# Optimization experiments

Measured on AMD Instinct MI355X. Metric: run time of the kernel, lower is better.

Reference implementation:

```python
import jax, jax.numpy as jnp
import numpy as np

N = 50000   # nodes
E = 800000  # edges (avg degree 16)
H = 64      # hidden feature dim (hidden_irreps = 64x0e)
A = 9       # attr dim = (lmax_attr+1)^2, lmax_attr=2
AMF = 1     # additional_message_features dim
L = 2       # num_layers (stacked SEGNNLayers)


def _swish(v):
    return v * jax.nn.sigmoid(v)


def _o3_tp(v, attr, W, V, b):
    # Channel-factorized (uvu-style) attribute-conditioned tensor product:
    # linear map of features, gated per-channel by a linear map of the
    # steerable attribute (spherical harmonics), plus bias.
    return (v @ W) * (attr @ V) + b


def setup_inputs() -> dict:
    key = jax.random.key(0)
    ks = jax.random.split(key, 18)
    sc = lambda fan_in: 1.0 / np.sqrt(fan_in)
    inp = {
        "x": jax.random.normal(ks[0], (N, H), jnp.float32),
        "edge_attr": jax.random.normal(ks[1], (E, A), jnp.float32),
        "node_attr": jax.random.normal(ks[2], (N, A), jnp.float32),
        "amf": jax.random.normal(ks[3], (E, AMF), jnp.float32),
        "Wm1": jax.random.normal(ks[4], (L, 2 * H + AMF, H), jnp.float32) * sc(2 * H + AMF),
        "Vm1": jax.random.normal(ks[5], (L, A, H), jnp.float32) * sc(A),
        "bm1": jnp.zeros((L, H), jnp.float32),
        "Wm2": jax.random.normal(ks[6], (L, H, H), jnp.float32) * sc(H),
        "Vm2": jax.random.normal(ks[7], (L, A, H), jnp.float32) * sc(A),
        "bm2": jnp.zeros((L, H), jnp.float32),
        "Wu1": jax.random.normal(ks[8], (L, 2 * H, H), jnp.float32) * sc(2 * H),
        "Vu1": jax.random.normal(ks[9], (L, A, H), jnp.float32) * sc(A),
        "bu1": jnp.zeros((L, H), jnp.float32),
        "Wu2": jax.random.normal(ks[10], (L, H, H), jnp.float32) * sc(H),
        "Vu2": jax.random.normal(ks[11], (L, A, H), jnp.float32) * sc(A),
        "bu2": jnp.zeros((L, H), jnp.float32),
        "edge_index": jax.random.randint(ks[12], (2, E), 0, N, jnp.int64),
    }
    return inp


def reference(x, edge_attr, node_attr, amf,
              Wm1, Vm1, bm1, Wm2, Vm2, bm2,
              Wu1, Vu1, bu1, Wu2, Vu2, bu2,
              edge_index):
    src = edge_index[0]  # x_j source
    dst = edge_index[1]  # x_i target / aggregation index
    for l in range(L):
        # --- message: gather, concat, TP-SwishGate x2 ---
        x_i = x[dst]                                   # [E, H]
        x_j = x[src]                                   # [E, H]
        m_in = jnp.concatenate([x_i, x_j, amf], -1)    # [E, 2H+AMF]
        m = _swish(_o3_tp(m_in, edge_attr, Wm1[l], Vm1[l], bm1[l]))
        m = _swish(_o3_tp(m, edge_attr, Wm2[l], Vm2[l], bm2[l]))
        # --- aggregate: scatter-add messages to target nodes ---
        agg = jax.ops.segment_sum(m, dst, num_segments=N)  # [N, H]
        # --- update: concat, TP-SwishGate, TP, residual blend ---
        u_in = jnp.concatenate([x, agg], -1)           # [N, 2H]
        u = _swish(_o3_tp(u_in, node_attr, Wu1[l], Vu1[l], bu1[l]))
        u = _o3_tp(u, node_attr, Wu2[l], Vu2[l], bu2[l])
        x = 0.7 * x + 0.3 * u
    return x
```

## Files before the change

### kernel.cpp

```cpp
#include <hip/hip_runtime.h>
#include <hip/hip_bf16.h>

#define NN 50000
#define NE 800000
#define H  64
#define AD 9

typedef __attribute__((ext_vector_type(8)))  short short8;
typedef __attribute__((ext_vector_type(16))) float f32x16;
typedef unsigned int uint;
typedef unsigned short ushort;

union U8 { short8 v; uint u[4]; ushort s[8]; };

__device__ __forceinline__ f32x16 MFMA(short8 a, short8 b, f32x16 c) {
    return __builtin_amdgcn_mfma_f32_32x32x16_bf16(a, b, c, 0, 0, 0);
}

__device__ __forceinline__ ushort f2bf(float v) {
    __hip_bfloat16 b = __float2bfloat16(v);
    return *(ushort*)&b;
}
__device__ __forceinline__ uint pkbf(float a, float b) {
    uint r;
    asm volatile("v_cvt_pk_bf16_f32 %0, %1, %2" : "=v"(r) : "v"(a), "v"(b));
    return r;
}
__device__ __forceinline__ float bflo(uint u) { return __uint_as_float(u << 16); }
__device__ __forceinline__ float bfhi(uint u) { return __uint_as_float(u & 0xffff0000u); }

__device__ __forceinline__ float swish_fast(float v) {
    return v * __builtin_amdgcn_rcpf(1.f + __expf(-v));
}

__device__ __forceinline__ void xhalf(uint& a, uint& b) {
    asm("v_permlane32_swap_b32 %0, %1" : "+v"(a), "+v"(b));
}

__device__ __forceinline__ void pack16(const float* y, short8* out) {
    #pragma unroll
    for (int g = 0; g < 2; ++g) {
        uint c0 = pkbf(y[g*8+0], y[g*8+1]);
        uint c1 = pkbf(y[g*8+2], y[g*8+3]);
        uint c2 = pkbf(y[g*8+4], y[g*8+5]);
        uint c3 = pkbf(y[g*8+6], y[g*8+7]);
        xhalf(c0, c2);
        xhalf(c1, c3);
        U8 q; q.u[0] = c0; q.u[1] = c1; q.u[2] = c2; q.u[3] = c3;
        out[g] = q.v;
    }
}

__global__ void prep_x(const float* __restrict__ x, ushort* __restrict__ xb) {
    int t = blockIdx.x * 256 + threadIdx.x;
    if (t >= NN * H / 8) return;
    const float* p = x + (size_t)t * 8;
    U8 o;
    #pragma unroll
    for (int j = 0; j < 8; ++j) o.s[j] = f2bf(p[j]);
    *(short8*)(xb + (size_t)t * 8) = o.v;
}

__global__ void prep_w(const float* __restrict__ Wm1, const float* __restrict__ Vm1,
                       const float* __restrict__ Wm2, const float* __restrict__ Vm2,
                       const float* __restrict__ Wu1, const float* __restrict__ Vu1,
                       const float* __restrict__ Wu2, const float* __restrict__ Vu2,
                       ushort* __restrict__ wbE, ushort* __restrict__ wbN) {
    int t = blockIdx.x * 256 + threadIdx.x;
    float v = 0.f;
    if (t < 2 * 17408) {
        int l = t / 17408, o = t % 17408;
        if (o < 10752)      { int h = o / 168, k = o % 168;            if (k < 129) v = Wm1[l*8256 + k*64 + h]; }
        else if (o < 15360) { int o2 = o-10752; int h = o2/72, k = o2%72; if (k < 64)  v = Wm2[l*4096 + k*64 + h]; }
        else if (o < 16384) { int o2 = o-15360; int h = o2/16, a = o2%16; if (a < 9)   v = Vm1[l*576 + a*64 + h]; }
        else                { int o2 = o-16384; int h = o2/16, a = o2%16; if (a < 9)   v = Vm2[l*576 + a*64 + h]; }
        wbE[t] = f2bf(v);
    } else if (t < 2 * 17408 + 2 * 15360) {
        int u = t - 2 * 17408;
        int l = u / 15360, o = u % 15360;
        if (o < 8704)       { int h = o / 136, k = o % 136;            if (k < 128) v = Wu1[l*8192 + k*64 + h]; }
        else if (o < 13312) { int o2 = o-8704;  int h = o2/72, k = o2%72; if (k < 64)  v = Wu2[l*4096 + k*64 + h]; }
        else if (o < 14336) { int o2 = o-13312; int h = o2/16, a = o2%16; if (a < 9)   v = Vu1[l*576 + a*64 + h]; }
        else                { int o2 = o-14336; int h = o2/16, a = o2%16; if (a < 9)   v = Vu2[l*576 + a*64 + h]; }
        wbN[u] = f2bf(v);
    }
}

__global__ void hist_k(const int* __restrict__ ei, int* __restrict__ cnt) {
    int t = blockIdx.x * 256 + threadIdx.x;
    if (t < NE) atomicAdd(&cnt[ei[NE + t]], 1);
}

__global__ void scan1_k(const int* __restrict__ cnt, int* __restrict__ partial,
                        int* __restrict__ btot) {
    __shared__ int sh[256];
    const int b = blockIdx.x, tid = threadIdx.x, i = b * 256 + tid;
    int c = cnt[i];
    sh[tid] = c; __syncthreads();
    int run = c;
    for (int off = 1; off < 256; off <<= 1) {
        int t = (tid >= off) ? sh[tid - off] : 0;
        __syncthreads();
        run += t; sh[tid] = run; __syncthreads();
    }
    partial[i] = run - c;
    if (tid == 255) btot[b] = run;
}

__global__ void scan2_k(const int* __restrict__ btot, int* __restrict__ boff) {
    __shared__ int sh[256];
    const int tid = threadIdx.x;
    int c = (tid < 200) ? btot[tid] : 0;
    sh[tid] = c; __syncthreads();
    int run = c;
    for (int off = 1; off < 256; off <<= 1) {
        int t = (tid >= off) ? sh[tid - off] : 0;
        __syncthreads();
        run += t; sh[tid] = run; __syncthreads();
    }
    boff[tid] = run - c;
}

__global__ void scan3_k(const int* __restrict__ partial, const int* __restrict__ boff,
                        int* __restrict__ cursor) {
    int b = blockIdx.x, i = b * 256 + threadIdx.x;
    if (i < NN) cursor[i] = partial[i] + boff[b];
}

__global__ void fill_k(const int* __restrict__ ei, const float* __restrict__ edge_attr,
                       const float* __restrict__ amf, int* __restrict__ cursor,
                       int* __restrict__ srcS, int* __restrict__ dstS,
                       uint4* __restrict__ eaLo, uint2* __restrict__ eaHi) {
    int e = blockIdx.x * 256 + threadIdx.x;
    if (e >= NE) return;
    const int dst = ei[NE + e], src = ei[e];
    const int pos = atomicAdd(&cursor[dst], 1);
    srcS[pos] = src; dstS[pos] = dst;
    float ea[AD];
    #pragma unroll
    for (int a = 0; a < AD; ++a) ea[a] = edge_attr[(size_t)e * AD + a];
    uint4 lo;
    lo.x = pkbf(ea[0], ea[1]); lo.y = pkbf(ea[2], ea[3]);
    lo.z = pkbf(ea[4], ea[5]); lo.w = pkbf(ea[6], ea[7]);
    eaLo[pos] = lo;
    uint2 hw;
    hw.x = pkbf(ea[8], 0.f); hw.y = pkbf(amf[e], 0.f);
    eaHi[pos] = hw;
}

struct M2Pack { short8 v[4]; };

__device__ __forceinline__ M2Pack msg_compute(
    const short8 bx[8], uint4 elo, uint2 ehi,
    const ushort* __restrict__ W1T, const ushort* __restrict__ wb,
    const short8 aW2[4][2], const short8 aV1[2], const short8 aV2[2],
    const float* __restrict__ b1, const float* __restrict__ b2,
    int l31, int hi) {
    U8 bea;
    bea.u[0] = hi ? ehi.x : elo.x;
    bea.u[1] = hi ? 0u : elo.y;
    bea.u[2] = hi ? 0u : elo.z;
    bea.u[3] = hi ? 0u : elo.w;

    f32x16 gA0 = {}, gA1 = {};
    gA0 = MFMA(aV1[0], bea.v, gA0);
    gA1 = MFMA(aV1[1], bea.v, gA1);

    f32x16 mA0 = {}, mA1 = {};
    #pragma unroll
    for (int s = 0; s < 8; ++s) {
        short8 a0 = *(const short8*)(W1T + l31 * 168 + s * 16 + hi * 8);
        short8 a1 = *(const short8*)(W1T + (l31 + 32) * 168 + s * 16 + hi * 8);
        mA0 = MFMA(a0, bx[s], mA0);
        mA1 = MFMA(a1, bx[s], mA1);
    }
    {
        U8 ba;
        ba.u[0] = hi ? 0u : ehi.y;
        ba.u[1] = 0; ba.u[2] = 0; ba.u[3] = 0;
        short8 a0 = *(const short8*)(W1T + l31 * 168 + 128 + hi * 8);
        short8 a1 = *(const short8*)(W1T + (l31 + 32) * 168 + 128 + hi * 8);
        mA0 = MFMA(a0, ba.v, mA0);
        mA1 = MFMA(a1, ba.v, mA1);
    }

    short8 bm[4];
    #pragma unroll
    for (int m = 0; m < 2; ++m) {
        const f32x16 mc = m ? mA1 : mA0;
        const f32x16 gc = m ? gA1 : gA0;
        float y[16];
        #pragma unroll
        for (int r = 0; r < 16; ++r) {
            int h0 = (r & 3) + 8 * (r >> 2) + 32 * m;
            float bb = hi ? b1[h0 + 4] : b1[h0];
            y[r] = swish_fast(fmaf(mc[r], gc[r], bb));
        }
        pack16(y, &bm[2 * m]);
    }

    f32x16 h0a = {}, h1a = {};
    h0a = MFMA(aV2[0], bea.v, h0a);
    h1a = MFMA(aV2[1], bea.v, h1a);
    f32x16 p0 = {}, p1 = {};
    #pragma unroll
    for (int s = 0; s < 4; ++s) {
        p0 = MFMA(aW2[s][0], bm[s], p0);
        p1 = MFMA(aW2[s][1], bm[s], p1);
    }

    M2Pack out;
    #pragma unroll
    for (int m = 0; m < 2; ++m) {
        const f32x16 mc = m ? p1 : p0;
        const f32x16 gc = m ? h1a : h0a;
        float y[16];
        #pragma unroll
        for (int r = 0; r < 16; ++r) {
            int h0 = (r & 3) + 8 * (r >> 2) + 32 * m;
            float bb = hi ? b2[h0 + 4] : b2[h0];
            y[r] = swish_fast(fmaf(mc[r], gc[r], bb));
        }
        pack16(y, &out.v[2 * m]);
    }
    return out;
}

__device__ __forceinline__ void gather_x(short8 bx[8], const ushort* __restrict__ xbf,
                                         int dst, int src, int hi) {
    const ushort* xd = xbf + (size_t)dst * H;
    const ushort* xs = xbf + (size_t)src * H;
    #pragma unroll
    for (int s = 0; s < 8; ++s)
        bx[s] = *(const short8*)((s < 4 ? xd : xs) + (s & 3) * 16 + hi * 8);
}

__device__ __forceinline__ void seg_reduce(const ushort* __restrict__ M2, int dst,
                                           float* __restrict__ agg, int lane) {
    float acc = 0.f;
    int cur = __builtin_amdgcn_readlane(dst, 0);
    #pragma unroll
    for (int r = 0; r < 32; ++r) {
        float v = bflo((uint)M2[r * 68 + lane]);
        int d = __builtin_amdgcn_readlane(dst, r);
        if (d != cur) {
            atomicAdd(&agg[(size_t)cur * H + lane], acc);
            acc = 0.f; cur = d;
        }
        acc += v;
    }
    atomicAdd(&agg[(size_t)cur * H + lane], acc);
}

__global__ __launch_bounds__(256, 4) void edge_mfma(
    const ushort* __restrict__ xbf, const uint4* __restrict__ eaLo,
    const uint2* __restrict__ eaHi, const int* __restrict__ srcS,
    const int* __restrict__ dstS, const ushort* __restrict__ wb,
    const float* __restrict__ b1, const float* __restrict__ b2,
    float* __restrict__ agg) {
    __shared__ __align__(16) ushort lds[10752 + 4 * 32 * 68];
    {
        const uint4* s4 = (const uint4*)wb;
        uint4* d4 = (uint4*)lds;
        for (int i = threadIdx.x; i < 1344; i += 256) d4[i] = s4[i];
    }
    __syncthreads();
    const ushort* W1T = lds;

    const int lane = threadIdx.x & 63;
    const int wv   = threadIdx.x >> 6;
    const int hi   = lane >> 5;
    const int l31  = lane & 31;
    ushort* M2 = lds + 10752 + wv * (32 * 68);

    const int i0 = blockIdx.x * 256 + wv * 64 + l31;
    const int i1 = i0 + 32;

    const int dst0 = dstS[i0], src0 = srcS[i0];
    const int dst1 = dstS[i1], src1 = srcS[i1];
    const uint4 elo0 = eaLo[i0], elo1 = eaLo[i1];
    const uint2 ehi0 = eaHi[i0], ehi1 = eaHi[i1];

    short8 aW2[4][2], aV1[2], aV2[2];
    #pragma unroll
    for (int m = 0; m < 2; ++m) {
        int r = l31 + 32 * m;
        aV1[m] = *(const short8*)(wb + 15360 + r * 16 + hi * 8);
        aV2[m] = *(const short8*)(wb + 16384 + r * 16 + hi * 8);
        #pragma unroll
        for (int s = 0; s < 4; ++s)
            aW2[s][m] = *(const short8*)(wb + 10752 + r * 72 + s * 16 + hi * 8);
    }

    short8 bx0[8];
    gather_x(bx0, xbf, dst0, src0, hi);
    M2Pack p0 = msg_compute(bx0, elo0, ehi0, W1T, wb, aW2, aV1, aV2, b1, b2, l31, hi);

    short8 bx1[8];
    gather_x(bx1, xbf, dst1, src1, hi);

    #pragma unroll
    for (int j = 0; j < 4; ++j)
        *(short8*)(M2 + l31 * 68 + j * 16 + hi * 8) = p0.v[j];
    seg_reduce(M2, dst0, agg, lane);

    M2Pack p1 = msg_compute(bx1, elo1, ehi1, W1T, wb, aW2, aV1, aV2, b1, b2, l31, hi);
    #pragma unroll
    for (int j = 0; j < 4; ++j)
        *(short8*)(M2 + l31 * 68 + j * 16 + hi * 8) = p1.v[j];
    seg_reduce(M2, dst1, agg, lane);
}

__global__ __launch_bounds__(256, 4) void node_mfma(
    const ushort* __restrict__ xbf, const float* __restrict__ agg,
    const float* __restrict__ node_attr, const ushort* __restrict__ wb,
    const float* __restrict__ b1, const float* __restrict__ b2,
    ushort* __restrict__ xnext, float* __restrict__ outf, int last) {
    __shared__ __align__(16) ushort lds[8704];
    {
        const uint4* s4 = (const uint4*)wb;
        uint4* d4 = (uint4*)lds;
        for (int i = threadIdx.x; i < 1088; i += 256) d4[i] = s4[i];
    }
    __syncthreads();
    const ushort* W1T = lds;

    const int lane = threadIdx.x & 63;
    const int wv   = threadIdx.x >> 6;
    const int hi   = lane >> 5;
    const int l31  = lane & 31;
    const int n    = blockIdx.x * 128 + wv * 32 + l31;
    const int nc   = n < NN ? n : NN - 1;

    short8 aW2[4][2], aV1[2], aV2[2];
    #pragma unroll
    for (int m = 0; m < 2; ++m) {
        int r = l31 + 32 * m;
        aV1[m] = *(const short8*)(wb + 13312 + r * 16 + hi * 8);
        aV2[m] = *(const short8*)(wb + 14336 + r * 16 + hi * 8);
        #pragma unroll
        for (int s = 0; s < 4; ++s)
            aW2[s][m] = *(const short8*)(wb + 8704 + r * 72 + s * 16 + hi * 8);
    }

    float na[AD];
    #pragma unroll
    for (int a = 0; a < AD; ++a) na[a] = node_attr[(size_t)nc * AD + a];

    U8 bna;
    {
        uint g0 = pkbf(na[0], na[1]), g1 = pkbf(na[2], na[3]);
        uint g2 = pkbf(na[4], na[5]), g3 = pkbf(na[6], na[7]);
        uint g8 = pkbf(na[8], 0.f);
        bna.u[0] = hi ? g8 : g0;
        bna.u[1] = hi ? 0u : g1;
        bna.u[2] = hi ? 0u : g2;
        bna.u[3] = hi ? 0u : g3;
    }
    f32x16 gA0 = {}, gA1 = {};
    gA0 = MFMA(aV1[0], bna.v, gA0);
    gA1 = MFMA(aV1[1], bna.v, gA1);

    f32x16 mA0 = {}, mA1 = {};
    #pragma unroll
    for (int s = 0; s < 8; ++s) {
        short8 bx;
        if (s < 4) {
            bx = *(const short8*)(xbf + (size_t)nc * H + s * 16 + hi * 8);
        } else {
            const float* ap = agg + (size_t)nc * H + (s - 4) * 16 + hi * 8;
            float4 u0 = *(const float4*)ap;
            float4 u1 = *(const float4*)(ap + 4);
            U8 q;
            q.u[0] = pkbf(u0.x, u0.y); q.u[1] = pkbf(u0.z, u0.w);
            q.u[2] = pkbf(u1.x, u1.y); q.u[3] = pkbf(u1.z, u1.w);
            bx = q.v;
        }
        short8 a0 = *(const short8*)(W1T + l31 * 136 + s * 16 + hi * 8);
        short8 a1 = *(const short8*)(W1T + (l31 + 32) * 136 + s * 16 + hi * 8);
        mA0 = MFMA(a0, bx, mA0);
        mA1 = MFMA(a1, bx, mA1);
    }

    short8 bm[4];
    #pragma unroll
    for (int m = 0; m < 2; ++m) {
        const f32x16 mc = m ? mA1 : mA0;
        const f32x16 gc = m ? gA1 : gA0;
        float y[16];
        #pragma unroll
        for (int r = 0; r < 16; ++r) {
            int h0 = (r & 3) + 8 * (r >> 2) + 32 * m;
            float bb = hi ? b1[h0 + 4] : b1[h0];
            y[r] = swish_fast(fmaf(mc[r], gc[r], bb));
        }
        pack16(y, &bm[2 * m]);
    }

    f32x16 h0a = {}, h1a = {};
    h0a = MFMA(aV2[0], bna.v, h0a);
    h1a = MFMA(aV2[1], bna.v, h1a);
    f32x16 p0 = {}, p1 = {};
    #pragma unroll
    for (int s = 0; s < 4; ++s) {
        p0 = MFMA(aW2[s][0], bm[s], p0);
        p1 = MFMA(aW2[s][1], bm[s], p1);
    }

    #pragma unroll
    for (int m = 0; m < 2; ++m) {
        const f32x16 mc = m ? p1 : p0;
        const f32x16 gc = m ? h1a : h0a;
        float y[16];
        #pragma unroll
        for (int r = 0; r < 16; ++r) {
            int h0 = (r & 3) + 8 * (r >> 2) + 32 * m;
            float bb = hi ? b2[h0 + 4] : b2[h0];
            y[r] = fmaf(mc[r], gc[r], bb);
        }
        #pragma unroll
        for (int g = 0; g < 2; ++g) {
            uint c0 = pkbf(y[g*8+0], y[g*8+1]);
            uint c1 = pkbf(y[g*8+2], y[g*8+3]);
            uint c2 = pkbf(y[g*8+4], y[g*8+5]);
            uint c3 = pkbf(y[g*8+6], y[g*8+7]);
            xhalf(c0, c2);
            xhalf(c1, c3);
            int goff = (2*m + g) * 16 + hi * 8;
            U8 xb; xb.v = *(const short8*)(xbf + (size_t)nc * H + goff);
            float o[8];
            uint cc[4] = {c0, c1, c2, c3};
            #pragma unroll
            for (int j = 0; j < 4; ++j) {
                o[2*j]   = 0.7f * bflo((uint)xb.u[j]) + 0.3f * bflo(cc[j]);
                o[2*j+1] = 0.7f * bfhi((uint)xb.u[j]) + 0.3f * bfhi(cc[j]);
            }
            if (n < NN) {
                if (last) {
                    float4 w0 = {o[0], o[1], o[2], o[3]};
                    float4 w1 = {o[4], o[5], o[6], o[7]};
                    *(float4*)(outf + (size_t)n * H + goff)     = w0;
                    *(float4*)(outf + (size_t)n * H + goff + 4) = w1;
                } else {
                    U8 q;
                    #pragma unroll
                    for (int j = 0; j < 4; ++j) q.u[j] = pkbf(o[2*j], o[2*j+1]);
                    *(short8*)(xnext + (size_t)n * H + goff) = q.v;
                }
            }
        }
    }
}

extern "C" void kernel_launch(void* const* d_in, const int* in_sizes, int n_in,
                              void* d_out, int out_size, void* d_ws, size_t ws_size,
                              hipStream_t stream) {
    const float* x         = (const float*)d_in[0];
    const float* edge_attr = (const float*)d_in[1];
    const float* node_attr = (const float*)d_in[2];
    const float* amf       = (const float*)d_in[3];
    const float* Wm1 = (const float*)d_in[4];
    const float* Vm1 = (const float*)d_in[5];
    const float* bm1 = (const float*)d_in[6];
    const float* Wm2 = (const float*)d_in[7];
    const float* Vm2 = (const float*)d_in[8];
    const float* bm2 = (const float*)d_in[9];
    const float* Wu1 = (const float*)d_in[10];
    const float* Vu1 = (const float*)d_in[11];
    const float* bu1 = (const float*)d_in[12];
    const float* Wu2 = (const float*)d_in[13];
    const float* Vu2 = (const float*)d_in[14];
    const float* bu2 = (const float*)d_in[15];
    const int*   ei  = (const int*)d_in[16];

    float* out = (float*)d_out;
    float* agg = (float*)d_out;

    ushort* xbf0 = (ushort*)d_ws;
    ushort* xbf1 = xbf0 + (size_t)NN * H;
    ushort* wbE  = xbf1 + (size_t)NN * H;
    ushort* wbN  = wbE + 2 * 17408;
    int* cnt     = (int*)(wbN + 2 * 15360);
    int* btot    = cnt + 51200;
    int* boff    = btot + 256;
    int* partial = boff + 256;
    int* cursor  = partial + 51200;
    int* srcS    = cursor + 50048;
    int* dstS    = srcS + NE;
    uint4* eaLo  = (uint4*)(dstS + NE);
    uint2* eaHi  = (uint2*)(eaLo + NE);

    prep_x<<<(NN * H / 8 + 255) / 256, 256, 0, stream>>>(x, xbf0);
    prep_w<<<256, 256, 0, stream>>>(Wm1, Vm1, Wm2, Vm2, Wu1, Vu1, Wu2, Vu2, wbE, wbN);

    hipMemsetAsync(cnt, 0, 51200 * sizeof(int), stream);
    hist_k<<<(NE + 255) / 256, 256, 0, stream>>>(ei, cnt);
    scan1_k<<<200, 256, 0, stream>>>(cnt, partial, btot);
    scan2_k<<<1, 256, 0, stream>>>(btot, boff);
    scan3_k<<<200, 256, 0, stream>>>(partial, boff, cursor);
    fill_k<<<(NE + 255) / 256, 256, 0, stream>>>(ei, edge_attr, amf, cursor,
                                                 srcS, dstS, eaLo, eaHi);

    for (int l = 0; l < 2; ++l) {
        const ushort* xb = (l == 0) ? xbf0 : xbf1;
        hipMemsetAsync(agg, 0, (size_t)NN * H * sizeof(float), stream);
        edge_mfma<<<NE / 256, 256, 0, stream>>>(
            xb, eaLo, eaHi, srcS, dstS, wbE + (size_t)l * 17408,
            bm1 + l * H, bm2 + l * H, agg);
        node_mfma<<<(NN + 127) / 128, 256, 0, stream>>>(
            xb, agg, node_attr, wbN + (size_t)l * 15360,
            bu1 + l * H, bu2 + l * H, xbf1, out, (l == 1) ? 1 : 0);
    }
}
```

Baseline: 312.5 us.

## Register-level segment reduction, packed edge indices, fused prep and XCD swizzle

Transposes the second message MFMA so each lane holds one channel across edges, enabling a ballot-driven in-register segmented sum that replaces the LDS staging buffer and serial reduction. Packs src/dst into ushort2 and edge hi-attributes into one uint to cut index/attribute bandwidth, raises edge-kernel occupancy hint, adds an XCD-aware block remap, and fuses the two prep kernels into one launch. The 16-bit indices rely on node count fitting in 65535, and the per-segment masked sums add ALU work when segments are short.

```diff
diff --git a/kernel.cpp b/kernel.cpp
--- a/kernel.cpp
+++ b/kernel.cpp
@@ -51,22 +51,24 @@
     }
 }
 
-__global__ void prep_x(const float* __restrict__ x, ushort* __restrict__ xb) {
-    int t = blockIdx.x * 256 + threadIdx.x;
-    if (t >= NN * H / 8) return;
-    const float* p = x + (size_t)t * 8;
-    U8 o;
-    #pragma unroll
-    for (int j = 0; j < 8; ++j) o.s[j] = f2bf(p[j]);
-    *(short8*)(xb + (size_t)t * 8) = o.v;
-}
-
-__global__ void prep_w(const float* __restrict__ Wm1, const float* __restrict__ Vm1,
-                       const float* __restrict__ Wm2, const float* __restrict__ Vm2,
-                       const float* __restrict__ Wu1, const float* __restrict__ Vu1,
-                       const float* __restrict__ Wu2, const float* __restrict__ Vu2,
-                       ushort* __restrict__ wbE, ushort* __restrict__ wbN) {
-    int t = blockIdx.x * 256 + threadIdx.x;
+__global__ void prep_all(const float* __restrict__ x, ushort* __restrict__ xb,
+                         const float* __restrict__ Wm1, const float* __restrict__ Vm1,
+                         const float* __restrict__ Wm2, const float* __restrict__ Vm2,
+                         const float* __restrict__ Wu1, const float* __restrict__ Vu1,
+                         const float* __restrict__ Wu2, const float* __restrict__ Vu2,
+                         ushort* __restrict__ wbE, ushort* __restrict__ wbN) {
+    const int b = blockIdx.x;
+    if (b < 1563) {
+        int t = b * 256 + threadIdx.x;
+        if (t >= NN * H / 8) return;
+        const float* p = x + (size_t)t * 8;
+        U8 o;
+        #pragma unroll
+        for (int j = 0; j < 8; ++j) o.s[j] = f2bf(p[j]);
+        *(short8*)(xb + (size_t)t * 8) = o.v;
+        return;
+    }
+    int t = (b - 1563) * 256 + threadIdx.x;
     float v = 0.f;
     if (t < 2 * 17408) {
         int l = t / 17408, o = t % 17408;
@@ -129,13 +131,14 @@
 
 __global__ void fill_k(const int* __restrict__ ei, const float* __restrict__ edge_attr,
                        const float* __restrict__ amf, int* __restrict__ cursor,
-                       int* __restrict__ srcS, int* __restrict__ dstS,
-                       uint4* __restrict__ eaLo, uint2* __restrict__ eaHi) {
+                       ushort2* __restrict__ nbrS, uint4* __restrict__ eaLo,
+                       uint* __restrict__ eaHi) {
     int e = blockIdx.x * 256 + threadIdx.x;
     if (e >= NE) return;
     const int dst = ei[NE + e], src = ei[e];
     const int pos = atomicAdd(&cursor[dst], 1);
-    srcS[pos] = src; dstS[pos] = dst;
+    ushort2 nd; nd.x = (ushort)src; nd.y = (ushort)dst;
+    nbrS[pos] = nd;
     float ea[AD];
     #pragma unroll
     for (int a = 0; a < AD; ++a) ea[a] = edge_attr[(size_t)e * AD + a];
@@ -143,21 +146,19 @@
     lo.x = pkbf(ea[0], ea[1]); lo.y = pkbf(ea[2], ea[3]);
     lo.z = pkbf(ea[4], ea[5]); lo.w = pkbf(ea[6], ea[7]);
     eaLo[pos] = lo;
-    uint2 hw;
-    hw.x = pkbf(ea[8], 0.f); hw.y = pkbf(amf[e], 0.f);
-    eaHi[pos] = hw;
-}
-
-struct M2Pack { short8 v[4]; };
-
-__device__ __forceinline__ M2Pack msg_compute(
-    const short8 bx[8], uint4 elo, uint2 ehi,
-    const ushort* __restrict__ W1T, const ushort* __restrict__ wb,
+    eaHi[pos] = pkbf(ea[8], amf[e]);
+}
+
+struct YPair { f32x16 a, b; };
+
+__device__ __forceinline__ YPair msg_compute(
+    const short8 bx[8], uint4 elo, uint ehi,
+    const ushort* __restrict__ W1T,
     const short8 aW2[4][2], const short8 aV1[2], const short8 aV2[2],
-    const float* __restrict__ b1, const float* __restrict__ b2,
+    const float* __restrict__ b1, float bias2_0, float bias2_1,
     int l31, int hi) {
     U8 bea;
-    bea.u[0] = hi ? ehi.x : elo.x;
+    bea.u[0] = hi ? (ehi & 0xffffu) : elo.x;
     bea.u[1] = hi ? 0u : elo.y;
     bea.u[2] = hi ? 0u : elo.z;
     bea.u[3] = hi ? 0u : elo.w;
@@ -176,7 +177,7 @@
     }
     {
         U8 ba;
-        ba.u[0] = hi ? 0u : ehi.y;
+        ba.u[0] = hi ? 0u : (ehi >> 16);
         ba.u[1] = 0; ba.u[2] = 0; ba.u[3] = 0;
         short8 a0 = *(const short8*)(W1T + l31 * 168 + 128 + hi * 8);
         short8 a1 = *(const short8*)(W1T + (l31 + 32) * 168 + 128 + hi * 8);
@@ -199,29 +200,21 @@
         pack16(y, &bm[2 * m]);
     }
 
-    f32x16 h0a = {}, h1a = {};
-    h0a = MFMA(aV2[0], bea.v, h0a);
-    h1a = MFMA(aV2[1], bea.v, h1a);
+    f32x16 g2a = {}, g2b = {};
+    g2a = MFMA(bea.v, aV2[0], g2a);
+    g2b = MFMA(bea.v, aV2[1], g2b);
     f32x16 p0 = {}, p1 = {};
     #pragma unroll
     for (int s = 0; s < 4; ++s) {
-        p0 = MFMA(aW2[s][0], bm[s], p0);
-        p1 = MFMA(aW2[s][1], bm[s], p1);
-    }
-
-    M2Pack out;
-    #pragma unroll
-    for (int m = 0; m < 2; ++m) {
-        const f32x16 mc = m ? p1 : p0;
-        const f32x16 gc = m ? h1a : h0a;
-        float y[16];
-        #pragma unroll
-        for (int r = 0; r < 16; ++r) {
-            int h0 = (r & 3) + 8 * (r >> 2) + 32 * m;
-            float bb = hi ? b2[h0 + 4] : b2[h0];
-            y[r] = swish_fast(fmaf(mc[r], gc[r], bb));
-        }
-        pack16(y, &out.v[2 * m]);
+        p0 = MFMA(bm[s], aW2[s][0], p0);
+        p1 = MFMA(bm[s], aW2[s][1], p1);
+    }
+
+    YPair out;
+    #pragma unroll
+    for (int r = 0; r < 16; ++r) {
+        out.a[r] = swish_fast(fmaf(p0[r], g2a[r], bias2_0));
+        out.b[r] = swish_fast(fmaf(p1[r], g2b[r], bias2_1));
     }
     return out;
 }
@@ -235,30 +228,39 @@
         bx[s] = *(const short8*)((s < 4 ? xd : xs) + (s & 3) * 16 + hi * 8);
 }
 
-__device__ __forceinline__ void seg_reduce(const ushort* __restrict__ M2, int dst,
-                                           float* __restrict__ agg, int lane) {
-    float acc = 0.f;
-    int cur = __builtin_amdgcn_readlane(dst, 0);
-    #pragma unroll
-    for (int r = 0; r < 32; ++r) {
-        float v = bflo((uint)M2[r * 68 + lane]);
-        int d = __builtin_amdgcn_readlane(dst, r);
-        if (d != cur) {
-            atomicAdd(&agg[(size_t)cur * H + lane], acc);
-            acc = 0.f; cur = d;
+__device__ __forceinline__ void reduce_write(const YPair& y, int dst,
+                                             float* __restrict__ agg,
+                                             int lane, int l31, int hi) {
+    int dp = __shfl_up(dst, 1);
+    bool nb = (l31 != 0) && (dst != dp);
+    uint mm = (uint)__ballot(nb);
+    int lo = 0;
+    while (lo < 32) {
+        int nx = mm ? (int)__builtin_ctz(mm) : 32;
+        mm &= mm - 1;
+        float s0 = 0.f, s1 = 0.f;
+        #pragma unroll
+        for (int r = 0; r < 16; ++r) {
+            int e = (r & 3) + 8 * (r >> 2) + 4 * hi;
+            bool in = ((uint)(e - lo) < (uint)(nx - lo));
+            s0 += in ? y.a[r] : 0.f;
+            s1 += in ? y.b[r] : 0.f;
         }
-        acc += v;
-    }
-    atomicAdd(&agg[(size_t)cur * H + lane], acc);
-}
-
-__global__ __launch_bounds__(256, 4) void edge_mfma(
+        s0 += __shfl_xor(s0, 32);
+        s1 += __shfl_xor(s1, 32);
+        int dseg = __builtin_amdgcn_readlane(dst, lo);
+        atomicAdd(&agg[(size_t)dseg * H + lane], hi ? s1 : s0);
+        lo = nx;
+    }
+}
+
+__global__ __launch_bounds__(256, 5) void edge_mfma(
     const ushort* __restrict__ xbf, const uint4* __restrict__ eaLo,
-    const uint2* __restrict__ eaHi, const int* __restrict__ srcS,
-    const int* __restrict__ dstS, const ushort* __restrict__ wb,
+    const uint* __restrict__ eaHi, const ushort2* __restrict__ nbrS,
+    const ushort* __restrict__ wb,
     const float* __restrict__ b1, const float* __restrict__ b2,
     float* __restrict__ agg) {
-    __shared__ __align__(16) ushort lds[10752 + 4 * 32 * 68];
+    __shared__ __align__(16) ushort lds[10752];
     {
         const uint4* s4 = (const uint4*)wb;
         uint4* d4 = (uint4*)lds;
@@ -271,15 +273,21 @@
     const int wv   = threadIdx.x >> 6;
     const int hi   = lane >> 5;
     const int l31  = lane & 31;
-    ushort* M2 = lds + 10752 + wv * (32 * 68);
-
-    const int i0 = blockIdx.x * 256 + wv * 64 + l31;
+
+    const int nwg = gridDim.x;
+    const int q = nwg >> 3, rr = nwg & 7;
+    const int xcd = blockIdx.x & 7, idx = blockIdx.x >> 3;
+    const int swz = (xcd < rr) ? (xcd * (q + 1) + idx)
+                               : (rr * (q + 1) + (xcd - rr) * q + idx);
+
+    const int i0 = swz * 256 + wv * 64 + l31;
     const int i1 = i0 + 32;
 
-    const int dst0 = dstS[i0], src0 = srcS[i0];
-    const int dst1 = dstS[i1], src1 = srcS[i1];
+    const ushort2 nd0 = nbrS[i0], nd1 = nbrS[i1];
+    const int src0 = nd0.x, dst0 = nd0.y;
+    const int src1 = nd1.x, dst1 = nd1.y;
     const uint4 elo0 = eaLo[i0], elo1 = eaLo[i1];
-    const uint2 ehi0 = eaHi[i0], ehi1 = eaHi[i1];
+    const uint  ehi0 = eaHi[i0], ehi1 = eaHi[i1];
 
     short8 aW2[4][2], aV1[2], aV2[2];
     #pragma unroll
@@ -292,23 +300,22 @@
             aW2[s][m] = *(const short8*)(wb + 10752 + r * 72 + s * 16 + hi * 8);
     }
 
+    const float bias2_0 = b2[l31];
+    const float bias2_1 = b2[l31 + 32];
+
     short8 bx0[8];
     gather_x(bx0, xbf, dst0, src0, hi);
-    M2Pack p0 = msg_compute(bx0, elo0, ehi0, W1T, wb, aW2, aV1, aV2, b1, b2, l31, hi);
+    YPair y0 = msg_compute(bx0, elo0, ehi0, W1T, aW2, aV1, aV2,
+                           b1, bias2_0, bias2_1, l31, hi);
 
     short8 bx1[8];
     gather_x(bx1, xbf, dst1, src1, hi);
 
-    #pragma unroll
-    for (int j = 0; j < 4; ++j)
-        *(short8*)(M2 + l31 * 68 + j * 16 + hi * 8) = p0.v[j];
-    seg_reduce(M2, dst0, agg, lane);
-
-    M2Pack p1 = msg_compute(bx1, elo1, ehi1, W1T, wb, aW2, aV1, aV2, b1, b2, l31, hi);
-    #pragma unroll
-    for (int j = 0; j < 4; ++j)
-        *(short8*)(M2 + l31 * 68 + j * 16 + hi * 8) = p1.v[j];
-    seg_reduce(M2, dst1, agg, lane);
+    reduce_write(y0, dst0, agg, lane, l31, hi);
+
+    YPair y1 = msg_compute(bx1, elo1, ehi1, W1T, aW2, aV1, aV2,
+                           b1, bias2_0, bias2_1, l31, hi);
+    reduce_write(y1, dst1, agg, lane, l31, hi);
 }
 
 __global__ __launch_bounds__(256, 4) void node_mfma(
@@ -476,22 +483,21 @@
     float* out = (float*)d_out;
     float* agg = (float*)d_out;
 
-    ushort* xbf0 = (ushort*)d_ws;
-    ushort* xbf1 = xbf0 + (size_t)NN * H;
-    ushort* wbE  = xbf1 + (size_t)NN * H;
-    ushort* wbN  = wbE + 2 * 17408;
-    int* cnt     = (int*)(wbN + 2 * 15360);
-    int* btot    = cnt + 51200;
-    int* boff    = btot + 256;
-    int* partial = boff + 256;
-    int* cursor  = partial + 51200;
-    int* srcS    = cursor + 50048;
-    int* dstS    = srcS + NE;
-    uint4* eaLo  = (uint4*)(dstS + NE);
-    uint2* eaHi  = (uint2*)(eaLo + NE);
-
-    prep_x<<<(NN * H / 8 + 255) / 256, 256, 0, stream>>>(x, xbf0);
-    prep_w<<<256, 256, 0, stream>>>(Wm1, Vm1, Wm2, Vm2, Wu1, Vu1, Wu2, Vu2, wbE, wbN);
+    ushort* xbf0  = (ushort*)d_ws;
+    ushort* xbf1  = xbf0 + (size_t)NN * H;
+    ushort* wbE   = xbf1 + (size_t)NN * H;
+    ushort* wbN   = wbE + 2 * 17408;
+    uint4*  eaLo  = (uint4*)(wbN + 2 * 15360);
+    uint*   eaHi  = (uint*)(eaLo + NE);
+    ushort2* nbrS = (ushort2*)(eaHi + NE);
+    int* cnt      = (int*)(nbrS + NE);
+    int* btot     = cnt + 51200;
+    int* boff     = btot + 256;
+    int* partial  = boff + 256;
+    int* cursor   = partial + 51200;
+
+    prep_all<<<1563 + 256, 256, 0, stream>>>(x, xbf0, Wm1, Vm1, Wm2, Vm2,
+                                             Wu1, Vu1, Wu2, Vu2, wbE, wbN);
 
     hipMemsetAsync(cnt, 0, 51200 * sizeof(int), stream);
     hist_k<<<(NE + 255) / 256, 256, 0, stream>>>(ei, cnt);
@@ -499,13 +505,13 @@
     scan2_k<<<1, 256, 0, stream>>>(btot, boff);
     scan3_k<<<200, 256, 0, stream>>>(partial, boff, cursor);
     fill_k<<<(NE + 255) / 256, 256, 0, stream>>>(ei, edge_attr, amf, cursor,
-                                                 srcS, dstS, eaLo, eaHi);
+                                                 nbrS, eaLo, eaHi);
 
     for (int l = 0; l < 2; ++l) {
         const ushort* xb = (l == 0) ? xbf0 : xbf1;
         hipMemsetAsync(agg, 0, (size_t)NN * H * sizeof(float), stream);
         edge_mfma<<<NE / 256, 256, 0, stream>>>(
-            xb, eaLo, eaHi, srcS, dstS, wbE + (size_t)l * 17408,
+            xb, eaLo, eaHi, nbrS, wbE + (size_t)l * 17408,
             bm1 + l * H, bm2 + l * H, agg);
         node_mfma<<<(NN + 127) / 128, 256, 0, stream>>>(
             xb, agg, node_attr, wbN + (size_t)l * 15360,
```

Measured after the change: 369.5 us. 18.2% more time.
